# Kernel tuning notes

Measured on AMD Instinct MI355X. Metric: run time of the kernel, lower is better.

## Reference

```python
import jax, jax.numpy as jnp
import numpy as np

N_ITEM = 80000
N_USER = 20000
D = 128
N_REL = 3
E = 1600000  # edges per relation (~avg degree 16 over N=100000 nodes)


def setup_inputs() -> dict:
    key = jax.random.key(0)
    ks = jax.random.split(key, 10)
    N = N_ITEM + N_USER
    s = 1.0 / np.sqrt(D).astype(np.float32)
    return {
        "h_item": jax.random.normal(ks[0], (N_ITEM, D), jnp.float32),
        "h_user": jax.random.normal(ks[1], (N_USER, D), jnp.float32),
        "W_rel": jax.random.normal(ks[2], (N_REL, D, D), jnp.float32) * s,
        "W_item": jax.random.normal(ks[3], (D, D), jnp.float32) * s,
        "b_item": jax.random.normal(ks[4], (D,), jnp.float32) * s,
        "W_user": jax.random.normal(ks[5], (D, D), jnp.float32) * s,
        "b_user": jax.random.normal(ks[6], (D,), jnp.float32) * s,
        "vals": jax.random.uniform(ks[7], (N_REL, E), jnp.float32),
        "rows": jax.random.randint(ks[8], (N_REL, E), 0, N, jnp.int32),
        "cols": jax.random.randint(ks[9], (N_REL, E), 0, N, jnp.int32),
    }


def reference(h_item, h_user, W_rel, W_item, b_item, W_user, b_user, vals, rows, cols):
    N_i = h_item.shape[0]
    N = N_i + h_user.shape[0]
    h_all = jnp.concatenate([h_item, h_user], axis=0)  # [N, D]
    msg = jnp.zeros_like(h_all)
    # loop over small fixed set of relations (structurally distinct weights)
    for r in range(W_rel.shape[0]):
        hr = h_all @ W_rel[r].T                      # lin_r[r](h_all), bias=False
        # sparse.mm(A_r, hr): gather source rows, scale by edge value, scatter-add to dest
        m = jax.ops.segment_sum(hr[cols[r]] * vals[r][:, None], rows[r], num_segments=N)
        msg = msg + m
    h_item_out = jax.nn.relu((msg[:N_i] + h_item) @ W_item.T + b_item)
    h_user_out = jax.nn.relu((msg[N_i:] + h_user) @ W_user.T + b_user)
    return h_item_out, h_user_out
```

## Files before the change

kernel.cpp:

```cpp
#include <hip/hip_runtime.h>
#include <cstdint>

#define D 128
#define BK 64
#define CAP 1216
#define CHUNK 4096
#define NBK_MAX 1568

typedef short   bf8_t    __attribute__((ext_vector_type(8)));
typedef float   f4_t     __attribute__((ext_vector_type(4)));
typedef unsigned short u8x16_t __attribute__((ext_vector_type(8)));

__device__ __forceinline__ float bf2f(unsigned short u) {
    unsigned v = ((unsigned)u) << 16; float f; __builtin_memcpy(&f, &v, 4); return f;
}
__device__ __forceinline__ unsigned short f2bf(float f) {
    unsigned v; __builtin_memcpy(&v, &f, 4);
    v = v + 0x7FFFu + ((v >> 16) & 1u);
    return (unsigned short)(v >> 16);
}

__global__ __launch_bounds__(256) void place_kernel(
    const int* __restrict__ rows, const int* __restrict__ cols,
    const float* __restrict__ vals, int* __restrict__ bcnt3,
    uint2* __restrict__ ev0, int E, int nbk, int relBase, size_t evStride)
{
    __shared__ int cnt[NBK_MAX];
    __shared__ int base[NBK_MAX];
    const int rel = relBase + blockIdx.y;
    const int* rowsR = rows + (size_t)rel * E;
    const int* colsR = cols + (size_t)rel * E;
    const float* valsR = vals + (size_t)rel * E;
    int* bcnt = bcnt3 + (size_t)rel * NBK_MAX * 16;
    uint2* ev = ev0 + (size_t)rel * evStride;

    const int tid = threadIdx.x;
    const int e0 = blockIdx.x * CHUNK;
    const int ecnt = min(CHUNK, E - e0);

    for (int b = tid; b < nbk; b += 256) cnt[b] = 0;
    __syncthreads();
    for (int i = tid; i < ecnt; i += 256)
        atomicAdd(&cnt[rowsR[e0 + i] >> 6], 1);
    __syncthreads();
    for (int b = tid; b < nbk; b += 256) {
        int c = cnt[b];
        base[b] = c ? atomicAdd(&bcnt[b * 16], c) : 0;
        cnt[b] = 0;
    }
    __syncthreads();
    for (int i = tid; i < ecnt; i += 256) {
        int r = rowsR[e0 + i];
        int b = r >> 6;
        int pos = base[b] + atomicAdd(&cnt[b], 1);
        if (pos < CAP)
            ev[(size_t)b * CAP + pos] =
                make_uint2(((unsigned)(r & 63) << 17) | (unsigned)colsR[e0 + i],
                           __float_as_uint(valsR[e0 + i]));
    }
}

__global__ __launch_bounds__(256) void sort_kernel(
    const int* __restrict__ bcnt3, uint2* __restrict__ ev0,
    int* __restrict__ rstart3, int* __restrict__ rend3,
    int N, int relBase, size_t evStride)
{
    __shared__ uint2 se[CAP];
    __shared__ int hist[BK], cur[BK];
    const int rel = relBase + blockIdx.y;
    const int tid = threadIdx.x;
    const int b = blockIdx.x;
    const int cnt = min(bcnt3[(size_t)rel * NBK_MAX * 16 + b * 16], CAP);
    uint2* ev = ev0 + (size_t)rel * evStride;
    int* rstart = rstart3 + (size_t)rel * N;
    int* rend   = rend3   + (size_t)rel * N;

    for (int i = tid; i < cnt; i += 256) se[i] = ev[(size_t)b * CAP + i];
    if (tid < BK) hist[tid] = 0;
    __syncthreads();
    for (int i = tid; i < cnt; i += 256)
        atomicAdd(&hist[se[i].x >> 17], 1);
    __syncthreads();
    if (tid < BK) {
        int x = hist[tid], orig = x;
        #pragma unroll
        for (int d = 1; d < 64; d <<= 1) {
            int y = __shfl_up(x, d);
            if (tid >= d) x += y;
        }
        cur[tid] = x - orig;
        int g = b * BK + tid;
        if (g < N) {
            rstart[g] = b * CAP + x - orig;
            rend[g]   = b * CAP + x;
        }
    }
    __syncthreads();
    for (int i = tid; i < cnt; i += 256) {
        uint2 x = se[i];
        int pos = atomicAdd(&cur[x.x >> 17], 1);
        ev[(size_t)b * CAP + pos] = make_uint2(x.x & 0x1FFFFu, x.y);
    }
}

template<int FIRST>
__global__ __launch_bounds__(256) void accum_row(
    const unsigned short* __restrict__ hr, const uint2* __restrict__ ev,
    const int* __restrict__ rstart, const int* __restrict__ rend,
    const float* __restrict__ h_item, const float* __restrict__ h_user,
    unsigned short* __restrict__ X, int N, int Ni)
{
    int row = blockIdx.x * 4 + (threadIdx.x >> 6);
    if (row >= N) return;
    const int lane = threadIdx.x & 63;
    int s = rstart[row], t = rend[row];

    float a0, a1;
    if (FIRST) {
        const float* hsrc = (row < Ni) ? h_item + (size_t)row * D
                                       : h_user + (size_t)(row - Ni) * D;
        float2 hv = *reinterpret_cast<const float2*>(hsrc + lane * 2);
        a0 = hv.x; a1 = hv.y;
    } else {
        if (s == t) return;
        ushort2 xv = *reinterpret_cast<const ushort2*>(X + (size_t)row * D + lane * 2);
        a0 = bf2f(xv.x); a1 = bf2f(xv.y);
    }

    int p = s;
    if (p + 8 <= t) {
        uint2 e[8];
        #pragma unroll
        for (int j = 0; j < 8; ++j) e[j] = ev[p + j];
        while (true) {
            ushort2 g[8];
            #pragma unroll
            for (int j = 0; j < 8; ++j)
                g[j] = *reinterpret_cast<const ushort2*>(
                    hr + ((size_t)e[j].x << 7) + lane * 2);
            int pn = p + 8;
            bool more = (pn + 8 <= t);
            uint2 f[8];
            if (more) {
                #pragma unroll
                for (int j = 0; j < 8; ++j) f[j] = ev[pn + j];
            }
            #pragma unroll
            for (int j = 0; j < 8; ++j) {
                float v = __uint_as_float(e[j].y);
                a0 = fmaf(v, bf2f(g[j].x), a0);
                a1 = fmaf(v, bf2f(g[j].y), a1);
            }
            p = pn;
            if (!more) break;
            #pragma unroll
            for (int j = 0; j < 8; ++j) e[j] = f[j];
        }
    }
    for (; p < t; ++p) {
        uint2 ee = ev[p];
        ushort2 g = *reinterpret_cast<const ushort2*>(
            hr + ((size_t)ee.x << 7) + lane * 2);
        a0 = fmaf(__uint_as_float(ee.y), bf2f(g.x), a0);
        a1 = fmaf(__uint_as_float(ee.y), bf2f(g.y), a1);
    }
    *reinterpret_cast<ushort2*>(X + (size_t)row * D + lane * 2) =
        make_ushort2(f2bf(a0), f2bf(a1));
}

template<int AMODE, int FINAL>
__global__ __launch_bounds__(256) void gemm128(
    const void* __restrict__ Aptr, const void* __restrict__ A2ptr,
    const float* __restrict__ Wf, const float* __restrict__ biasp,
    void* __restrict__ outp, int Ni, int Ntot, int Mvalid)
{
    __shared__ char LDS[2 * 128 * 272];
    char* As = LDS;
    char* Bs = LDS + 128 * 272;
    const int tid  = threadIdx.x;
    const int lane = tid & 63;
    const int wv   = tid >> 6;
    const int row0 = blockIdx.x * 128;

    #pragma unroll
    for (int i = 0; i < 8; ++i) {
        int idx = i * 256 + tid;
        int r = idx >> 4, u = idx & 15;
        const float* wp = Wf + r * D + u * 8;
        float4 w0 = *reinterpret_cast<const float4*>(wp);
        float4 w1 = *reinterpret_cast<const float4*>(wp + 4);
        u8x16_t us;
        us[0]=f2bf(w0.x); us[1]=f2bf(w0.y); us[2]=f2bf(w0.z); us[3]=f2bf(w0.w);
        us[4]=f2bf(w1.x); us[5]=f2bf(w1.y); us[6]=f2bf(w1.z); us[7]=f2bf(w1.w);
        *reinterpret_cast<u8x16_t*>(&Bs[r * 272 + u * 16]) = us;
    }
    #pragma unroll
    for (int i = 0; i < 8; ++i) {
        int idx = i * 256 + tid;
        int r = idx >> 4, u = idx & 15;
        int gr = row0 + r;
        u8x16_t us = {};
        if (AMODE == 0) {
            if (gr < Ntot) {
                const float* hp = (gr < Ni)
                    ? (const float*)Aptr  + (size_t)gr * D
                    : (const float*)A2ptr + (size_t)(gr - Ni) * D;
                float4 a0 = *reinterpret_cast<const float4*>(hp + u * 8);
                float4 a1 = *reinterpret_cast<const float4*>(hp + u * 8 + 4);
                us[0]=f2bf(a0.x); us[1]=f2bf(a0.y); us[2]=f2bf(a0.z); us[3]=f2bf(a0.w);
                us[4]=f2bf(a1.x); us[5]=f2bf(a1.y); us[6]=f2bf(a1.z); us[7]=f2bf(a1.w);
            }
        } else {
            us = *reinterpret_cast<const u8x16_t*>(
                (const unsigned short*)Aptr + (size_t)gr * D + u * 8);
        }
        *reinterpret_cast<u8x16_t*>(&As[r * 272 + u * 16]) = us;
    }
    __syncthreads();

    const int wm = wv >> 1, wn = wv & 1;
    f4_t acc[4][4] = {};

    #pragma unroll
    for (int kk = 0; kk < 4; ++kk) {
        const int ku = kk * 4 + (lane >> 4);
        bf8_t a[4], bfr[4];
        #pragma unroll
        for (int mi = 0; mi < 4; ++mi) {
            int r = wm * 64 + mi * 16 + (lane & 15);
            a[mi] = *reinterpret_cast<const bf8_t*>(&As[r * 272 + ku * 16]);
        }
        #pragma unroll
        for (int nj = 0; nj < 4; ++nj) {
            int r = wn * 64 + nj * 16 + (lane & 15);
            bfr[nj] = *reinterpret_cast<const bf8_t*>(&Bs[r * 272 + ku * 16]);
        }
        #pragma unroll
        for (int mi = 0; mi < 4; ++mi)
            #pragma unroll
            for (int nj = 0; nj < 4; ++nj)
                acc[mi][nj] = __builtin_amdgcn_mfma_f32_16x16x32_bf16(
                    a[mi], bfr[nj], acc[mi][nj], 0, 0, 0);
    }
    __syncthreads();

    if (FINAL == 0) {
        #pragma unroll
        for (int mi = 0; mi < 4; ++mi)
            #pragma unroll
            for (int nj = 0; nj < 4; ++nj)
                #pragma unroll
                for (int q = 0; q < 4; ++q) {
                    int r = wm * 64 + mi * 16 + (lane >> 4) * 4 + q;
                    int c = wn * 64 + nj * 16 + (lane & 15);
                    *reinterpret_cast<unsigned short*>(&As[r * 272 + c * 2]) =
                        f2bf(acc[mi][nj][q]);
                }
        __syncthreads();
        #pragma unroll
        for (int i = 0; i < 8; ++i) {
            int idx = i * 256 + tid;
            int r = idx >> 4, u = idx & 15;
            u8x16_t v = *reinterpret_cast<const u8x16_t*>(&As[r * 272 + u * 16]);
            *reinterpret_cast<u8x16_t*>(
                (unsigned short*)outp + (size_t)(row0 + r) * D + u * 8) = v;
        }
    } else {
        #pragma unroll
        for (int mi = 0; mi < 4; ++mi)
            #pragma unroll
            for (int nj = 0; nj < 4; ++nj)
                #pragma unroll
                for (int q = 0; q < 4; ++q) {
                    int r = wm * 64 + mi * 16 + (lane >> 4) * 4 + q;
                    int c = wn * 64 + nj * 16 + (lane & 15);
                    *reinterpret_cast<float*>(&LDS[r * 544 + c * 4]) = acc[mi][nj][q];
                }
        __syncthreads();
        #pragma unroll
        for (int i = 0; i < 16; ++i) {
            int idx = i * 256 + tid;
            int r = idx >> 5, u = idx & 31;
            int gr = row0 + r;
            if (gr < Mvalid) {
                f4_t v = *reinterpret_cast<const f4_t*>(&LDS[r * 544 + u * 16]);
                float4 bb = *reinterpret_cast<const float4*>(biasp + u * 4);
                v[0] = fmaxf(v[0] + bb.x, 0.f);
                v[1] = fmaxf(v[1] + bb.y, 0.f);
                v[2] = fmaxf(v[2] + bb.z, 0.f);
                v[3] = fmaxf(v[3] + bb.w, 0.f);
                *reinterpret_cast<f4_t*>((float*)outp + (size_t)gr * D + u * 4) = v;
            }
        }
    }
}

extern "C" void kernel_launch(void* const* d_in, const int* in_sizes, int n_in,
                              void* d_out, int out_size, void* d_ws, size_t ws_size,
                              hipStream_t stream)
{
    const float* h_item = (const float*)d_in[0];
    const float* h_user = (const float*)d_in[1];
    const float* W_rel  = (const float*)d_in[2];
    const float* W_item = (const float*)d_in[3];
    const float* b_item = (const float*)d_in[4];
    const float* W_user = (const float*)d_in[5];
    const float* b_user = (const float*)d_in[6];
    const float* vals   = (const float*)d_in[7];
    const int*   rows   = (const int*)d_in[8];
    const int*   cols   = (const int*)d_in[9];

    const int Ni = in_sizes[0] / D;
    const int Nu = in_sizes[1] / D;
    const int N  = Ni + Nu;
    const int NR = in_sizes[2] / (D * D);
    const int E  = in_sizes[7] / NR;
    const int MPAD = ((N + 127) / 128) * 128;
    const int NBKP = MPAD / BK;
    const int nbk  = (N + BK - 1) / BK;

    auto au = [](size_t x) { return (x + 255) & ~(size_t)255; };
    const size_t xB   = au((size_t)MPAD * D * 2);
    const size_t hrB  = au((size_t)MPAD * D * 2);
    const size_t bcB  = au((size_t)3 * NBK_MAX * 16 * 4);
    const size_t rsB  = au((size_t)3 * N * 4);
    const size_t evB1 = au((size_t)NBKP * CAP * sizeof(uint2));

    const bool merged = ws_size >= xB + hrB + bcB + 2 * rsB + 3 * evB1;

    char* p = (char*)d_ws;
    unsigned short* X  = (unsigned short*)p; p += xB;
    unsigned short* hr = (unsigned short*)p; p += hrB;
    int* bcnt3   = (int*)p;   p += bcB;
    int* rstart3 = (int*)p;   p += rsB;
    int* rend3   = (int*)p;   p += rsB;
    uint2* ev    = (uint2*)p;
    const size_t evStride = merged ? (size_t)NBKP * CAP : 0;
    float* out = (float*)d_out;

    const int pblocks = (E + CHUNK - 1) / CHUNK;

    hipMemsetAsync(bcnt3, 0, (size_t)3 * NBK_MAX * 16 * sizeof(int), stream);

    if (merged) {
        place_kernel<<<dim3(pblocks, 3), 256, 0, stream>>>(
            rows, cols, vals, bcnt3, ev, E, nbk, 0, evStride);
        sort_kernel<<<dim3(nbk, 3), 256, 0, stream>>>(
            bcnt3, ev, rstart3, rend3, N, 0, evStride);
    }

    for (int r = 0; r < NR; ++r) {
        if (!merged) {
            place_kernel<<<dim3(pblocks, 1), 256, 0, stream>>>(
                rows, cols, vals, bcnt3, ev, E, nbk, r, 0);
            sort_kernel<<<dim3(nbk, 1), 256, 0, stream>>>(
                bcnt3, ev, rstart3, rend3, N, r, 0);
        }
        gemm128<0, 0><<<MPAD / 128, 256, 0, stream>>>(
            h_item, h_user, W_rel + (size_t)r * D * D, nullptr, hr, Ni, N, 0);
        if (r == 0)
            accum_row<1><<<(N + 3) / 4, 256, 0, stream>>>(
                hr, ev + r * evStride, rstart3 + (size_t)r * N,
                rend3 + (size_t)r * N, h_item, h_user, X, N, Ni);
        else
            accum_row<0><<<(N + 3) / 4, 256, 0, stream>>>(
                hr, ev + r * evStride, rstart3 + (size_t)r * N,
                rend3 + (size_t)r * N, h_item, h_user, X, N, Ni);
    }

    gemm128<1, 1><<<(Ni + 127) / 128, 256, 0, stream>>>(
        X, nullptr, W_item, b_item, out, 0, 0, Ni);
    gemm128<1, 1><<<(MPAD - Ni) / 128, 256, 0, stream>>>(
        X + (size_t)Ni * D, nullptr, W_user, b_user, out + (size_t)Ni * D, 0, 0, Nu);
}
```

Before: 542.8 us.

## Replace atomic bucket placement with count/scan/write deterministic binning

The single place kernel, which reserved bucket slots with global atomics, becomes three stages. A count kernel writes per-chunk bucket histograms, a scan kernel computes exclusive offsets per bucket across chunks, and a write kernel scatters edges to precomputed positions using only shared-memory atomics. This drops the global atomic contention and the memset, and makes edge order within each bucket deterministic. It adds two launches per relation plus a histogram buffer, and it always processes one relation at a time in a single ev buffer instead of using the merged three-relation path.

```diff
diff --git a/kernel.cpp b/kernel.cpp
--- a/kernel.cpp
+++ b/kernel.cpp
@@ -5,7 +5,7 @@
 #define BK 64
 #define CAP 1216
 #define CHUNK 4096
-#define NBK_MAX 1568
+#define NBH 1568
 
 typedef short   bf8_t    __attribute__((ext_vector_type(8)));
 typedef float   f4_t     __attribute__((ext_vector_type(4)));
@@ -20,60 +20,83 @@
     return (unsigned short)(v >> 16);
 }
 
-__global__ __launch_bounds__(256) void place_kernel(
-    const int* __restrict__ rows, const int* __restrict__ cols,
-    const float* __restrict__ vals, int* __restrict__ bcnt3,
-    uint2* __restrict__ ev0, int E, int nbk, int relBase, size_t evStride)
-{
-    __shared__ int cnt[NBK_MAX];
-    __shared__ int base[NBK_MAX];
-    const int rel = relBase + blockIdx.y;
+__global__ __launch_bounds__(256) void count_kernel(
+    const int* __restrict__ rows, int* __restrict__ hist,
+    int E, int nbk, int nblk)
+{
+    __shared__ int cnt[NBH];
+    const int rel = blockIdx.y, blk = blockIdx.x, tid = threadIdx.x;
     const int* rowsR = rows + (size_t)rel * E;
-    const int* colsR = cols + (size_t)rel * E;
-    const float* valsR = vals + (size_t)rel * E;
-    int* bcnt = bcnt3 + (size_t)rel * NBK_MAX * 16;
-    uint2* ev = ev0 + (size_t)rel * evStride;
-
-    const int tid = threadIdx.x;
-    const int e0 = blockIdx.x * CHUNK;
+    const int e0 = blk * CHUNK;
     const int ecnt = min(CHUNK, E - e0);
 
-    for (int b = tid; b < nbk; b += 256) cnt[b] = 0;
+    for (int b = tid; b < NBH; b += 256) cnt[b] = 0;
     __syncthreads();
     for (int i = tid; i < ecnt; i += 256)
         atomicAdd(&cnt[rowsR[e0 + i] >> 6], 1);
     __syncthreads();
-    for (int b = tid; b < nbk; b += 256) {
-        int c = cnt[b];
-        base[b] = c ? atomicAdd(&bcnt[b * 16], c) : 0;
-        cnt[b] = 0;
-    }
+    int* hrow = hist + ((size_t)rel * nblk + blk) * NBH;
+    for (int b = tid; b < nbk; b += 256) hrow[b] = cnt[b];
+}
+
+__global__ __launch_bounds__(256) void scan_kernel(
+    int* __restrict__ hist, int* __restrict__ bcnt, int nbk, int nblk)
+{
+    const int rel = blockIdx.y;
+    const int b = blockIdx.x * 256 + threadIdx.x;
+    if (b >= nbk) return;
+    int* h = hist + (size_t)rel * nblk * NBH + b;
+    int o = 0;
+    int blk = 0;
+    for (; blk + 4 <= nblk; blk += 4) {
+        int v0 = h[(size_t)(blk + 0) * NBH];
+        int v1 = h[(size_t)(blk + 1) * NBH];
+        int v2 = h[(size_t)(blk + 2) * NBH];
+        int v3 = h[(size_t)(blk + 3) * NBH];
+        h[(size_t)(blk + 0) * NBH] = o; o += v0;
+        h[(size_t)(blk + 1) * NBH] = o; o += v1;
+        h[(size_t)(blk + 2) * NBH] = o; o += v2;
+        h[(size_t)(blk + 3) * NBH] = o; o += v3;
+    }
+    for (; blk < nblk; ++blk) {
+        int v = h[(size_t)blk * NBH]; h[(size_t)blk * NBH] = o; o += v;
+    }
+    bcnt[rel * NBH + b] = o;
+}
+
+__global__ __launch_bounds__(256) void write_kernel(
+    const int* __restrict__ rows, const int* __restrict__ cols,
+    const float* __restrict__ vals, const int* __restrict__ hist,
+    uint2* __restrict__ ev, int E, int nbk)
+{
+    __shared__ int cur[NBH];
+    const int blk = blockIdx.x, tid = threadIdx.x;
+    const int e0 = blk * CHUNK;
+    const int ecnt = min(CHUNK, E - e0);
+    const int* hrow = hist + (size_t)blk * NBH;
+
+    for (int b = tid; b < nbk; b += 256) cur[b] = hrow[b];
     __syncthreads();
     for (int i = tid; i < ecnt; i += 256) {
-        int r = rowsR[e0 + i];
+        int r = rows[e0 + i];
         int b = r >> 6;
-        int pos = base[b] + atomicAdd(&cnt[b], 1);
+        int pos = atomicAdd(&cur[b], 1);
         if (pos < CAP)
             ev[(size_t)b * CAP + pos] =
-                make_uint2(((unsigned)(r & 63) << 17) | (unsigned)colsR[e0 + i],
-                           __float_as_uint(valsR[e0 + i]));
+                make_uint2(((unsigned)(r & 63) << 17) | (unsigned)cols[e0 + i],
+                           __float_as_uint(vals[e0 + i]));
     }
 }
 
 __global__ __launch_bounds__(256) void sort_kernel(
-    const int* __restrict__ bcnt3, uint2* __restrict__ ev0,
-    int* __restrict__ rstart3, int* __restrict__ rend3,
-    int N, int relBase, size_t evStride)
+    const int* __restrict__ bcnt, uint2* __restrict__ ev,
+    int* __restrict__ rstart, int* __restrict__ rend, int N)
 {
     __shared__ uint2 se[CAP];
     __shared__ int hist[BK], cur[BK];
-    const int rel = relBase + blockIdx.y;
     const int tid = threadIdx.x;
     const int b = blockIdx.x;
-    const int cnt = min(bcnt3[(size_t)rel * NBK_MAX * 16 + b * 16], CAP);
-    uint2* ev = ev0 + (size_t)rel * evStride;
-    int* rstart = rstart3 + (size_t)rel * N;
-    int* rend   = rend3   + (size_t)rel * N;
+    const int cnt = min(bcnt[b], CAP);
 
     for (int i = tid; i < cnt; i += 256) se[i] = ev[(size_t)b * CAP + i];
     if (tid < BK) hist[tid] = 0;
@@ -316,56 +339,37 @@
     const int NR = in_sizes[2] / (D * D);
     const int E  = in_sizes[7] / NR;
     const int MPAD = ((N + 127) / 128) * 128;
-    const int NBKP = MPAD / BK;
     const int nbk  = (N + BK - 1) / BK;
+    const int nblk = (E + CHUNK - 1) / CHUNK;
 
     auto au = [](size_t x) { return (x + 255) & ~(size_t)255; };
-    const size_t xB   = au((size_t)MPAD * D * 2);
-    const size_t hrB  = au((size_t)MPAD * D * 2);
-    const size_t bcB  = au((size_t)3 * NBK_MAX * 16 * 4);
-    const size_t rsB  = au((size_t)3 * N * 4);
-    const size_t evB1 = au((size_t)NBKP * CAP * sizeof(uint2));
-
-    const bool merged = ws_size >= xB + hrB + bcB + 2 * rsB + 3 * evB1;
-
     char* p = (char*)d_ws;
-    unsigned short* X  = (unsigned short*)p; p += xB;
-    unsigned short* hr = (unsigned short*)p; p += hrB;
-    int* bcnt3   = (int*)p;   p += bcB;
-    int* rstart3 = (int*)p;   p += rsB;
-    int* rend3   = (int*)p;   p += rsB;
-    uint2* ev    = (uint2*)p;
-    const size_t evStride = merged ? (size_t)NBKP * CAP : 0;
+    unsigned short* X  = (unsigned short*)p; p += au((size_t)MPAD * D * 2);
+    unsigned short* hr = (unsigned short*)p; p += au((size_t)MPAD * D * 2);
+    uint2* ev          = (uint2*)p;          p += au((size_t)nbk * CAP * 8);
+    int*   hist        = (int*)p;            p += au((size_t)3 * nblk * NBH * 4);
+    int*   bcnt        = (int*)p;            p += au((size_t)3 * NBH * 4);
+    int*   rstart      = (int*)p;            p += au((size_t)N * 4);
+    int*   rend        = (int*)p;            p += au((size_t)N * 4);
     float* out = (float*)d_out;
 
-    const int pblocks = (E + CHUNK - 1) / CHUNK;
-
-    hipMemsetAsync(bcnt3, 0, (size_t)3 * NBK_MAX * 16 * sizeof(int), stream);
-
-    if (merged) {
-        place_kernel<<<dim3(pblocks, 3), 256, 0, stream>>>(
-            rows, cols, vals, bcnt3, ev, E, nbk, 0, evStride);
-        sort_kernel<<<dim3(nbk, 3), 256, 0, stream>>>(
-            bcnt3, ev, rstart3, rend3, N, 0, evStride);
-    }
+    count_kernel<<<dim3(nblk, 3), 256, 0, stream>>>(rows, hist, E, nbk, nblk);
+    scan_kernel<<<dim3((nbk + 255) / 256, 3), 256, 0, stream>>>(hist, bcnt, nbk, nblk);
 
     for (int r = 0; r < NR; ++r) {
-        if (!merged) {
-            place_kernel<<<dim3(pblocks, 1), 256, 0, stream>>>(
-                rows, cols, vals, bcnt3, ev, E, nbk, r, 0);
-            sort_kernel<<<dim3(nbk, 1), 256, 0, stream>>>(
-                bcnt3, ev, rstart3, rend3, N, r, 0);
-        }
+        write_kernel<<<nblk, 256, 0, stream>>>(
+            rows + (size_t)r * E, cols + (size_t)r * E, vals + (size_t)r * E,
+            hist + (size_t)r * nblk * NBH, ev, E, nbk);
+        sort_kernel<<<nbk, 256, 0, stream>>>(
+            bcnt + (size_t)r * NBH, ev, rstart, rend, N);
         gemm128<0, 0><<<MPAD / 128, 256, 0, stream>>>(
             h_item, h_user, W_rel + (size_t)r * D * D, nullptr, hr, Ni, N, 0);
         if (r == 0)
             accum_row<1><<<(N + 3) / 4, 256, 0, stream>>>(
-                hr, ev + r * evStride, rstart3 + (size_t)r * N,
-                rend3 + (size_t)r * N, h_item, h_user, X, N, Ni);
+                hr, ev, rstart, rend, h_item, h_user, X, N, Ni);
         else
             accum_row<0><<<(N + 3) / 4, 256, 0, stream>>>(
-                hr, ev + r * evStride, rstart3 + (size_t)r * N,
-                rend3 + (size_t)r * N, h_item, h_user, X, N, Ni);
+                hr, ev, rstart, rend, h_item, h_user, X, N, Ni);
     }
 
     gemm128<1, 1><<<(Ni + 127) / 128, 256, 0, stream>>>(
```

Measured after the change: 474.5 us. -12.6%, faster.
